# Kernel optimization log

Hardware: AMD Instinct MI355X
Metric: run time of the kernel (lower is better)

## Reference

```python
import jax, jax.numpy as jnp
import numpy as np

N = 262144      # total nodes across batched graphs
E = 4194304     # directed edges
G = 16384       # number of graphs
C = 26          # num_classes (ASL letters)


def gcn_layer(h, src, dst, W, b, n):
    """PyG GCNConv with improved=True (self-loop weight 2.0), symmetric norm."""
    h = h @ W  # [N, out]
    ones = jnp.ones(src.shape[0], h.dtype)
    deg = jax.ops.segment_sum(ones, dst, num_segments=n) + 2.0  # in-degree + improved self loop
    dis = jax.lax.rsqrt(deg)  # deg > 0 always (self loops)
    norm = dis[src] * dis[dst]  # [E]
    agg = jax.ops.segment_sum(norm[:, None] * h[src], dst, num_segments=n)
    agg = agg + (2.0 * dis * dis)[:, None] * h  # self-loop contribution (weight 2)
    return agg + b


def setup_inputs() -> dict:
    key = jax.random.key(0)
    ks = jax.random.split(key, 9)
    x = jax.random.normal(ks[0], (N, 3), dtype=jnp.float32)
    edge_index = jax.random.randint(ks[1], (2, E), 0, N, dtype=jnp.int64)
    batch = jnp.sort(jax.random.randint(ks[2], (N,), 0, G, dtype=jnp.int64))
    # GCNConv uses Glorot init on weight, zeros bias
    W1 = jax.random.normal(ks[3], (3, 16), dtype=jnp.float32) * (2.0 / (3 + 16)) ** 0.5
    b1 = jnp.zeros((16,), jnp.float32)
    W2 = jax.random.normal(ks[4], (16, 32), dtype=jnp.float32) * (2.0 / (16 + 32)) ** 0.5
    b2 = jnp.zeros((32,), jnp.float32)
    Wl = jax.random.normal(ks[5], (32, C), dtype=jnp.float32) * (1.0 / 32) ** 0.5
    bl = jax.random.normal(ks[6], (C,), dtype=jnp.float32) * 0.01
    return {"x": x, "edge_index": edge_index, "batch": batch,
            "W1": W1, "b1": b1, "W2": W2, "b2": b2, "Wl": Wl, "bl": bl}


def reference(x, edge_index, batch, W1, b1, W2, b2, Wl, bl):
    src, dst = edge_index[0], edge_index[1]
    n = x.shape[0]
    h = jax.nn.relu(gcn_layer(x, src, dst, W1, b1, n))
    h = jax.nn.relu(gcn_layer(h, src, dst, W2, b2, n))
    # global mean pool over graphs
    sums = jax.ops.segment_sum(h, batch, num_segments=G)           # [G, 32]
    cnts = jax.ops.segment_sum(jnp.ones(n, h.dtype), batch, num_segments=G)
    pooled = sums / jnp.maximum(cnts, 1.0)[:, None]
    return pooled @ Wl + bl  # [G, C]
```

## Files before the change

kernel.cpp:

```cpp
#include <hip/hip_runtime.h>
#include <hip/hip_fp16.h>

#define NN 262144
#define NE 4194304
#define NG 16384
#define NC 26
#define F1 16
#define F2 32
#define NB 512
#define BINCH 16384
#define SLOT 9728
#define KMAX 19

typedef __attribute__((ext_vector_type(2))) float floatx2;

#define ACCROW8(r) do { \
    floatx2 f_; \
    f_ = __builtin_amdgcn_cvt_pk_f32_fp8((int)(r).x, false); acc[0]  += f_.x; acc[1]  += f_.y; \
    f_ = __builtin_amdgcn_cvt_pk_f32_fp8((int)(r).x, true);  acc[2]  += f_.x; acc[3]  += f_.y; \
    f_ = __builtin_amdgcn_cvt_pk_f32_fp8((int)(r).y, false); acc[4]  += f_.x; acc[5]  += f_.y; \
    f_ = __builtin_amdgcn_cvt_pk_f32_fp8((int)(r).y, true);  acc[6]  += f_.x; acc[7]  += f_.y; \
    f_ = __builtin_amdgcn_cvt_pk_f32_fp8((int)(r).z, false); acc[8]  += f_.x; acc[9]  += f_.y; \
    f_ = __builtin_amdgcn_cvt_pk_f32_fp8((int)(r).z, true);  acc[10] += f_.x; acc[11] += f_.y; \
    f_ = __builtin_amdgcn_cvt_pk_f32_fp8((int)(r).w, false); acc[12] += f_.x; acc[13] += f_.y; \
    f_ = __builtin_amdgcn_cvt_pk_f32_fp8((int)(r).w, true);  acc[14] += f_.x; acc[15] += f_.y; \
} while (0)

__global__ __launch_bounds__(1024) void k_bin(const int* __restrict__ src,
                                              const int* __restrict__ dst,
                                              int* __restrict__ gcur,
                                              int* __restrict__ ebuf) {
    __shared__ int hist[NB];
    __shared__ int base[NB];
    int tid = threadIdx.x;
    if (tid < NB) hist[tid] = 0;
    __syncthreads();
    int e0 = blockIdx.x * BINCH;
    const int4* d4 = (const int4*)(dst + e0);
    const int4* s4 = (const int4*)(src + e0);
    int4 dreg[4];
    int4 preg[4];
    #pragma unroll
    for (int k = 0; k < 4; ++k) {
        int4 d = d4[tid + k * 1024];
        dreg[k] = d;
        int4 p;
        p.x = atomicAdd(&hist[d.x >> 9], 1);
        p.y = atomicAdd(&hist[d.y >> 9], 1);
        p.z = atomicAdd(&hist[d.z >> 9], 1);
        p.w = atomicAdd(&hist[d.w >> 9], 1);
        preg[k] = p;
    }
    __syncthreads();
    if (tid < NB) base[tid] = atomicAdd(&gcur[tid], hist[tid]);
    __syncthreads();
    #pragma unroll
    for (int k = 0; k < 4; ++k) {
        int4 d = dreg[k];
        int4 s = s4[tid + k * 1024];
        int4 p = preg[k];
        int b, idx;
        b = d.x >> 9; idx = base[b] + p.x;
        if (idx < SLOT) ebuf[b * SLOT + idx] = (s.x << 9) | (d.x & 511);
        b = d.y >> 9; idx = base[b] + p.y;
        if (idx < SLOT) ebuf[b * SLOT + idx] = (s.y << 9) | (d.y & 511);
        b = d.z >> 9; idx = base[b] + p.z;
        if (idx < SLOT) ebuf[b * SLOT + idx] = (s.z << 9) | (d.z & 511);
        b = d.w >> 9; idx = base[b] + p.w;
        if (idx < SLOT) ebuf[b * SLOT + idx] = (s.w << 9) | (d.w & 511);
    }
}

__global__ __launch_bounds__(512) void k_bucket(const int* __restrict__ gcur,
                                                const int* __restrict__ ebuf,
                                                const int* __restrict__ batch,
                                                const float* __restrict__ x,
                                                int* __restrict__ rowptr,
                                                int* __restrict__ rowend,
                                                int* __restrict__ csr_src,
                                                float* __restrict__ dis,
                                                uint2* __restrict__ xs,
                                                int* __restrict__ gcnt) {
    __shared__ int sdeg[512];
    __shared__ int srow[512];
    __shared__ int wsum[8];
    int tid = threadIdx.x;
    int lane = tid & 63;
    int wid = tid >> 6;
    int b = blockIdx.x;
    int n0 = b << 9;
    sdeg[tid] = 0;
    __syncthreads();
    int beg = b * SLOT;
    int cnt = gcur[b];
    if (cnt > SLOT) cnt = SLOT;
    int ev[KMAX];
    int pl[KMAX];
    #pragma unroll
    for (int k = 0; k < KMAX; ++k) {
        int j = tid + (k << 9);
        ev[k] = (j < cnt) ? ebuf[beg + j] : -1;
    }
    #pragma unroll
    for (int k = 0; k < KMAX; ++k)
        pl[k] = (ev[k] >= 0) ? atomicAdd(&sdeg[((unsigned)ev[k]) & 511u], 1) : 0;
    __syncthreads();
    int mydeg = sdeg[tid];
    int incl = mydeg;
    #pragma unroll
    for (int off = 1; off < 64; off <<= 1) {
        int v = __shfl_up(incl, off, 64);
        if (lane >= off) incl += v;
    }
    if (lane == 63) wsum[wid] = incl;
    __syncthreads();
    if (wid == 0) {
        int v = (lane < 8) ? wsum[lane] : 0;
        int s = v;
        #pragma unroll
        for (int off = 1; off < 8; off <<= 1) {
            int u = __shfl_up(s, off, 64);
            if (lane >= off) s += u;
        }
        if (lane < 8) wsum[lane] = s - v;
    }
    __syncthreads();
    int row = beg + wsum[wid] + incl - mydeg;
    srow[tid] = row;
    int n = n0 + tid;
    rowptr[n] = row;
    rowend[n] = row + mydeg;
    float ddn = rsqrtf((float)mydeg + 2.0f);
    dis[n] = ddn;
    float xv0 = x[3 * n], xv1 = x[3 * n + 1], xv2 = x[3 * n + 2];
    __half2 p0 = __floats2half2_rn(ddn * xv0, ddn * xv1);
    __half2 p1 = __floats2half2_rn(ddn * xv2, 0.0f);
    xs[n] = make_uint2(*(unsigned*)&p0, *(unsigned*)&p1);
    atomicAdd(&gcnt[batch[n]], 1);
    __syncthreads();
    #pragma unroll
    for (int k = 0; k < KMAX; ++k) {
        if (ev[k] >= 0) {
            unsigned p = (unsigned)ev[k];
            int dl = p & 511u;
            csr_src[srow[dl] + pl[k]] = (int)(p >> 9);
        }
    }
}

__global__ __launch_bounds__(256) void k_g1(const int* __restrict__ rowptr,
                                            const int* __restrict__ rowend,
                                            const int* __restrict__ csr_src,
                                            const float* __restrict__ dis,
                                            const uint2* __restrict__ xs,
                                            const float* __restrict__ W1,
                                            const float* __restrict__ b1,
                                            uint4* __restrict__ h1q) {
    __shared__ float sW1[3 * F1];
    __shared__ float sb1[F1];
    if (threadIdx.x < 3 * F1) sW1[threadIdx.x] = W1[threadIdx.x];
    if (threadIdx.x < F1) sb1[threadIdx.x] = b1[threadIdx.x];
    __syncthreads();
    int n = blockIdx.x * 256 + threadIdx.x;
    float dd = dis[n];
    int beg = rowptr[n], end = rowend[n];
    float a0 = 0.f, a1v = 0.f, a2 = 0.f;
    int e = beg;
    for (; e + 7 < end; e += 8) {
        int s0 = csr_src[e],   s1 = csr_src[e+1], s2 = csr_src[e+2], s3 = csr_src[e+3];
        int s4 = csr_src[e+4], s5 = csr_src[e+5], s6 = csr_src[e+6], s7 = csr_src[e+7];
        uint2 r0 = xs[s0], r1 = xs[s1], r2 = xs[s2], r3 = xs[s3];
        uint2 r4 = xs[s4], r5 = xs[s5], r6 = xs[s6], r7 = xs[s7];
        float2 f;
        f = __half22float2(*(__half2*)&r0.x); a0 += f.x; a1v += f.y;
        f = __half22float2(*(__half2*)&r0.y); a2 += f.x;
        f = __half22float2(*(__half2*)&r1.x); a0 += f.x; a1v += f.y;
        f = __half22float2(*(__half2*)&r1.y); a2 += f.x;
        f = __half22float2(*(__half2*)&r2.x); a0 += f.x; a1v += f.y;
        f = __half22float2(*(__half2*)&r2.y); a2 += f.x;
        f = __half22float2(*(__half2*)&r3.x); a0 += f.x; a1v += f.y;
        f = __half22float2(*(__half2*)&r3.y); a2 += f.x;
        f = __half22float2(*(__half2*)&r4.x); a0 += f.x; a1v += f.y;
        f = __half22float2(*(__half2*)&r4.y); a2 += f.x;
        f = __half22float2(*(__half2*)&r5.x); a0 += f.x; a1v += f.y;
        f = __half22float2(*(__half2*)&r5.y); a2 += f.x;
        f = __half22float2(*(__half2*)&r6.x); a0 += f.x; a1v += f.y;
        f = __half22float2(*(__half2*)&r6.y); a2 += f.x;
        f = __half22float2(*(__half2*)&r7.x); a0 += f.x; a1v += f.y;
        f = __half22float2(*(__half2*)&r7.y); a2 += f.x;
    }
    for (; e < end; ++e) {
        int s_ = csr_src[e];
        uint2 r = xs[s_];
        float2 lo = __half22float2(*(__half2*)&r.x), hi = __half22float2(*(__half2*)&r.y);
        a0 += lo.x; a1v += lo.y; a2 += hi.x;
    }
    {
        uint2 rn = xs[n];
        float2 lo = __half22float2(*(__half2*)&rn.x), hi = __half22float2(*(__half2*)&rn.y);
        a0 += 2.0f * lo.x; a1v += 2.0f * lo.y; a2 += 2.0f * hi.x;
    }
    float g0 = dd * a0, g1 = dd * a1v, g2 = dd * a2;
    float vals[F1];
    #pragma unroll
    for (int col = 0; col < F1; ++col) {
        float acc = sb1[col];
        acc += g0 * sW1[0 * F1 + col];
        acc += g1 * sW1[1 * F1 + col];
        acc += g2 * sW1[2 * F1 + col];
        vals[col] = dd * fmaxf(acc, 0.0f);
    }
    int d0 = 0, d1 = 0, d2 = 0, d3 = 0;
    d0 = __builtin_amdgcn_cvt_pk_fp8_f32(vals[0],  vals[1],  d0, false);
    d0 = __builtin_amdgcn_cvt_pk_fp8_f32(vals[2],  vals[3],  d0, true);
    d1 = __builtin_amdgcn_cvt_pk_fp8_f32(vals[4],  vals[5],  d1, false);
    d1 = __builtin_amdgcn_cvt_pk_fp8_f32(vals[6],  vals[7],  d1, true);
    d2 = __builtin_amdgcn_cvt_pk_fp8_f32(vals[8],  vals[9],  d2, false);
    d2 = __builtin_amdgcn_cvt_pk_fp8_f32(vals[10], vals[11], d2, true);
    d3 = __builtin_amdgcn_cvt_pk_fp8_f32(vals[12], vals[13], d3, false);
    d3 = __builtin_amdgcn_cvt_pk_fp8_f32(vals[14], vals[15], d3, true);
    h1q[n] = make_uint4((unsigned)d0, (unsigned)d1, (unsigned)d2, (unsigned)d3);
}

__global__ __launch_bounds__(256) void k_h2seg(const int* __restrict__ rowptr,
                                               const int* __restrict__ rowend,
                                               const int* __restrict__ csr_src,
                                               const float* __restrict__ dis,
                                               const uint4* __restrict__ h1q,
                                               const float* __restrict__ W2,
                                               const float* __restrict__ b2,
                                               const int* __restrict__ batch,
                                               float* __restrict__ gsum) {
    __shared__ float sW2[F1 * F2];
    __shared__ float sb2[F2];
    for (int i = threadIdx.x; i < F1 * F2; i += 256) sW2[i] = W2[i];
    if (threadIdx.x < F2) sb2[threadIdx.x] = b2[threadIdx.x];
    __syncthreads();
    int t = blockIdx.x * 256 + threadIdx.x;
    int n = t >> 2;
    int q = t & 3;
    int lane = threadIdx.x & 63;
    int islot = lane >> 2;
    float dd = dis[n];
    int beg = rowptr[n], end = rowend[n];
    float acc[F1];
    #pragma unroll
    for (int k = 0; k < F1; ++k) acc[k] = 0.0f;
    int e = beg + q;
    for (; e + 12 < end; e += 16) {
        int s0 = csr_src[e], s1 = csr_src[e + 4], s2 = csr_src[e + 8], s3 = csr_src[e + 12];
        uint4 r0 = h1q[s0];
        uint4 r1 = h1q[s1];
        uint4 r2 = h1q[s2];
        uint4 r3 = h1q[s3];
        ACCROW8(r0);
        ACCROW8(r1);
        ACCROW8(r2);
        ACCROW8(r3);
    }
    for (; e < end; e += 4) {
        int s_ = csr_src[e];
        uint4 r = h1q[s_];
        ACCROW8(r);
    }
    #pragma unroll
    for (int k = 0; k < F1; ++k) {
        acc[k] += __shfl_xor(acc[k], 1, 64);
        acc[k] += __shfl_xor(acc[k], 2, 64);
    }
    float av[F1];
    {
        uint4 rn = h1q[n];
        floatx2 f_;
        f_ = __builtin_amdgcn_cvt_pk_f32_fp8((int)rn.x, false); av[0]  = dd * (acc[0]  + 2.f * f_.x); av[1]  = dd * (acc[1]  + 2.f * f_.y);
        f_ = __builtin_amdgcn_cvt_pk_f32_fp8((int)rn.x, true);  av[2]  = dd * (acc[2]  + 2.f * f_.x); av[3]  = dd * (acc[3]  + 2.f * f_.y);
        f_ = __builtin_amdgcn_cvt_pk_f32_fp8((int)rn.y, false); av[4]  = dd * (acc[4]  + 2.f * f_.x); av[5]  = dd * (acc[5]  + 2.f * f_.y);
        f_ = __builtin_amdgcn_cvt_pk_f32_fp8((int)rn.y, true);  av[6]  = dd * (acc[6]  + 2.f * f_.x); av[7]  = dd * (acc[7]  + 2.f * f_.y);
        f_ = __builtin_amdgcn_cvt_pk_f32_fp8((int)rn.z, false); av[8]  = dd * (acc[8]  + 2.f * f_.x); av[9]  = dd * (acc[9]  + 2.f * f_.y);
        f_ = __builtin_amdgcn_cvt_pk_f32_fp8((int)rn.z, true);  av[10] = dd * (acc[10] + 2.f * f_.x); av[11] = dd * (acc[11] + 2.f * f_.y);
        f_ = __builtin_amdgcn_cvt_pk_f32_fp8((int)rn.w, false); av[12] = dd * (acc[12] + 2.f * f_.x); av[13] = dd * (acc[13] + 2.f * f_.y);
        f_ = __builtin_amdgcn_cvt_pk_f32_fp8((int)rn.w, true);  av[14] = dd * (acc[14] + 2.f * f_.x); av[15] = dd * (acc[15] + 2.f * f_.y);
    }
    float hv[8];
    #pragma unroll
    for (int j0 = 0; j0 < 8; ++j0) {
        int j = q * 8 + j0;
        float a_ = sb2[j];
        #pragma unroll
        for (int k = 0; k < F1; ++k) a_ += av[k] * sW2[k * F2 + j];
        hv[j0] = fmaxf(a_, 0.0f);
    }
    int g = batch[n];
    #pragma unroll
    for (int d_ = 1; d_ < 16; d_ <<= 1) {
        int sl = lane - 4 * d_;
        int gs = __shfl(g, sl, 64);
        #pragma unroll
        for (int j0 = 0; j0 < 8; ++j0) {
            float o = __shfl(hv[j0], sl, 64);
            if (islot >= d_ && gs == g) hv[j0] += o;
        }
    }
    int gn = __shfl(g, lane + 4, 64);
    bool endseg = (islot == 15) || (gn != g);
    if (endseg) {
        float* gr = gsum + (size_t)g * F2 + q * 8;
        #pragma unroll
        for (int j0 = 0; j0 < 8; ++j0) atomicAdd(gr + j0, hv[j0]);
    }
}

__global__ __launch_bounds__(256) void k_out2(const float* __restrict__ gsum,
                                              const int* __restrict__ gcnt,
                                              const float* __restrict__ Wl,
                                              const float* __restrict__ bl,
                                              float* __restrict__ out) {
    int t = blockIdx.x * 256 + threadIdx.x;
    if (t >= NG * NC) return;
    int g = t / NC, c = t - g * NC;
    float inv = 1.0f / fmaxf((float)gcnt[g], 1.0f);
    const float* gr = gsum + (size_t)g * F2;
    float acc = 0.0f;
    #pragma unroll
    for (int k = 0; k < F2; ++k) acc += gr[k] * Wl[k * NC + c];
    out[t] = acc * inv + bl[c];
}

extern "C" void kernel_launch(void* const* d_in, const int* in_sizes, int n_in,
                              void* d_out, int out_size, void* d_ws, size_t ws_size,
                              hipStream_t stream) {
    const float* x    = (const float*)d_in[0];
    const int*   ei   = (const int*)d_in[1];
    const int*   src  = ei;
    const int*   dst  = ei + NE;
    const int*   batch= (const int*)d_in[2];
    const float* W1   = (const float*)d_in[3];
    const float* b1   = (const float*)d_in[4];
    const float* W2   = (const float*)d_in[5];
    const float* b2   = (const float*)d_in[6];
    const float* Wl   = (const float*)d_in[7];
    const float* bl   = (const float*)d_in[8];
    float* out = (float*)d_out;

    int*   gcur   = (int*)d_ws;
    int*   gcnt   = gcur + NB;
    float* gsum   = (float*)(gcnt + NG);
    int*   rowptr = (int*)(gsum + (size_t)F2 * NG);
    int*   rowend = rowptr + NN;
    float* dis    = (float*)(rowend + NN);
    uint2* xs     = (uint2*)(dis + NN);
    int*   csr_src= (int*)(xs + NN);
    int*   ebuf   = csr_src + (size_t)NB * SLOT;
    uint4* h1q    = (uint4*)ebuf;

    size_t zero_elems = (size_t)NB + NG + (size_t)F2 * NG;
    hipMemsetAsync(d_ws, 0, zero_elems * sizeof(int), stream);

    k_bin    <<<NE / BINCH, 1024, 0, stream>>>(src, dst, gcur, ebuf);
    k_bucket <<<NB, 512, 0, stream>>>(gcur, ebuf, batch, x, rowptr, rowend, csr_src, dis, xs, gcnt);
    k_g1     <<<NN / 256, 256, 0, stream>>>(rowptr, rowend, csr_src, dis, xs, W1, b1, h1q);
    k_h2seg  <<<NN * 4 / 256, 256, 0, stream>>>(rowptr, rowend, csr_src, dis, h1q, W2, b2, batch, gsum);
    k_out2   <<<(NG * NC + 255) / 256, 256, 0, stream>>>(gsum, gcnt, Wl, bl, out);
}
```

Measured before the change: 167.7 us.

## Stage scattered edge writes through LDS for coalesced global stores

In the binning kernel, edges are first sorted by bucket into a 64KB shared-memory array using a local prefix scan over the bucket histogram. Each thread then binary-searches the local offsets to write contiguous runs to the global bucket buffer. The CSR build kernel likewise scatters into a shared array and copies it out linearly. The aim is to replace random scattered global stores with coalesced ones, at the cost of large LDS allocations that reduce occupancy, plus extra syncs and a binary search per element.

```diff
diff --git a/kernel.cpp b/kernel.cpp
--- a/kernel.cpp
+++ b/kernel.cpp
@@ -31,7 +31,10 @@
                                               int* __restrict__ gcur,
                                               int* __restrict__ ebuf) {
     __shared__ int hist[NB];
+    __shared__ int lstart[NB];
     __shared__ int base[NB];
+    __shared__ int wsum2[8];
+    __shared__ int eval[BINCH];
     int tid = threadIdx.x;
     if (tid < NB) hist[tid] = 0;
     __syncthreads();
@@ -52,22 +55,57 @@
         preg[k] = p;
     }
     __syncthreads();
-    if (tid < NB) base[tid] = atomicAdd(&gcur[tid], hist[tid]);
+    int myv = 0, incl = 0;
+    if (tid < NB) {
+        myv = hist[tid];
+        incl = myv;
+        #pragma unroll
+        for (int off = 1; off < 64; off <<= 1) {
+            int u = __shfl_up(incl, off, 64);
+            if ((tid & 63) >= off) incl += u;
+        }
+        if ((tid & 63) == 63) wsum2[tid >> 6] = incl;
+    }
+    __syncthreads();
+    if (tid < 64) {
+        int v8 = (tid < 8) ? wsum2[tid] : 0;
+        int s = v8;
+        #pragma unroll
+        for (int off = 1; off < 8; off <<= 1) {
+            int u = __shfl_up(s, off, 64);
+            if (tid >= off) s += u;
+        }
+        if (tid < 8) wsum2[tid] = s - v8;
+    }
+    __syncthreads();
+    if (tid < NB) {
+        lstart[tid] = wsum2[tid >> 6] + incl - myv;
+        base[tid] = atomicAdd(&gcur[tid], myv);
+    }
     __syncthreads();
     #pragma unroll
     for (int k = 0; k < 4; ++k) {
         int4 d = dreg[k];
         int4 s = s4[tid + k * 1024];
         int4 p = preg[k];
-        int b, idx;
-        b = d.x >> 9; idx = base[b] + p.x;
-        if (idx < SLOT) ebuf[b * SLOT + idx] = (s.x << 9) | (d.x & 511);
-        b = d.y >> 9; idx = base[b] + p.y;
-        if (idx < SLOT) ebuf[b * SLOT + idx] = (s.y << 9) | (d.y & 511);
-        b = d.z >> 9; idx = base[b] + p.z;
-        if (idx < SLOT) ebuf[b * SLOT + idx] = (s.z << 9) | (d.z & 511);
-        b = d.w >> 9; idx = base[b] + p.w;
-        if (idx < SLOT) ebuf[b * SLOT + idx] = (s.w << 9) | (d.w & 511);
+        int b;
+        b = d.x >> 9; eval[lstart[b] + p.x] = (s.x << 9) | (d.x & 511);
+        b = d.y >> 9; eval[lstart[b] + p.y] = (s.y << 9) | (d.y & 511);
+        b = d.z >> 9; eval[lstart[b] + p.z] = (s.z << 9) | (d.z & 511);
+        b = d.w >> 9; eval[lstart[b] + p.w] = (s.w << 9) | (d.w & 511);
+    }
+    __syncthreads();
+    for (int j = tid; j < BINCH; j += 1024) {
+        int v = eval[j];
+        int lo = 0, hi = NB - 1;
+        #pragma unroll
+        for (int it = 0; it < 9; ++it) {
+            int mid = (lo + hi + 1) >> 1;
+            if (lstart[mid] <= j) lo = mid; else hi = mid - 1;
+        }
+        int b = lo;
+        int idx = base[b] + (j - lstart[b]);
+        if (idx < SLOT) ebuf[b * SLOT + idx] = v;
     }
 }
 
@@ -82,8 +120,9 @@
                                                 uint2* __restrict__ xs,
                                                 int* __restrict__ gcnt) {
     __shared__ int sdeg[512];
-    __shared__ int srow[512];
+    __shared__ int lrow[512];
     __shared__ int wsum[8];
+    __shared__ int lcsr[SLOT];
     int tid = threadIdx.x;
     int lane = tid & 63;
     int wid = tid >> 6;
@@ -125,11 +164,11 @@
         if (lane < 8) wsum[lane] = s - v;
     }
     __syncthreads();
-    int row = beg + wsum[wid] + incl - mydeg;
-    srow[tid] = row;
+    int lr = wsum[wid] + incl - mydeg;
+    lrow[tid] = lr;
     int n = n0 + tid;
-    rowptr[n] = row;
-    rowend[n] = row + mydeg;
+    rowptr[n] = beg + lr;
+    rowend[n] = beg + lr + mydeg;
     float ddn = rsqrtf((float)mydeg + 2.0f);
     dis[n] = ddn;
     float xv0 = x[3 * n], xv1 = x[3 * n + 1], xv2 = x[3 * n + 2];
@@ -142,10 +181,12 @@
     for (int k = 0; k < KMAX; ++k) {
         if (ev[k] >= 0) {
             unsigned p = (unsigned)ev[k];
-            int dl = p & 511u;
-            csr_src[srow[dl] + pl[k]] = (int)(p >> 9);
-        }
-    }
+            lcsr[lrow[p & 511u] + pl[k]] = (int)(p >> 9);
+        }
+    }
+    __syncthreads();
+    for (int j = tid; j < cnt; j += 512)
+        csr_src[beg + j] = lcsr[j];
 }
 
 __global__ __launch_bounds__(256) void k_g1(const int* __restrict__ rowptr,
```

Result: faster. 146.5 us (-12.6%).
